# Kernel tuning notes

Hardware: AMD Instinct MI355X
Metric: run time of the kernel (lower is better)

The kernel has to match this reference:

```python
import jax, jax.numpy as jnp
import numpy as np

# HistogramQuantizer(percentile=99.99, gamma=0.99, n_bits=8, eps=0.0, act_decay=0.01), training mode
PERCENTILE = 99.99 / 100.0
GAMMA = 0.99
Q_MAX = float(2 ** (8 - 1) - 1)  # 127.0
EPS = 0.0
CLAMP_INIT = 100.0  # registered buffer initial value


def setup_inputs() -> dict:
    key = jax.random.key(0)
    x = jax.random.normal(key, (4, 4096, 4096), dtype=jnp.float32)
    return {"x": x}


def reference(x):
    x_abs = jnp.abs(x)
    # --- training-path percentile via full sort (quantile_from_sorted) ---
    flat = jnp.sort(x_abs.ravel())
    n = flat.size  # static
    k = int(round(PERCENTILE * n)) - 1
    clamp_value = flat[k]
    # EMA buffer update (side state; returned so the sort is not dead code)
    new_buffer = CLAMP_INIT * GAMMA + clamp_value * (1.0 - GAMMA)
    # --- fake quantization (Quantizer.forward with q_max=Q_MAX) ---
    # note: x_max/clamp_value only affects the backward mask, not the forward math
    scale = Q_MAX / jnp.maximum(jnp.max(x_abs), EPS)
    out = jnp.clip(jnp.round(x * scale), -Q_MAX, Q_MAX) / scale
    return out, new_buffer
```

## Files before the change

kernel.cpp:

```cpp
#include <hip/hip_runtime.h>
#include <math.h>

#define WS_MAXBITS 0
#define WS_SELBIN  1
#define WS_RANK    2
#define WS_HIST    4
#define HIST_WORDS 4096
#define WS_BMAX    4100
#define WS_CNT     5124
#define WS_CAND    6160
#define NBLK       1024
#define CAP        256

typedef float floatx4 __attribute__((ext_vector_type(4)));

extern "C" __global__ void __launch_bounds__(256)
k_max_hist(const float* __restrict__ x, long n, unsigned int* __restrict__ ws) {
    __shared__ unsigned int lhist[HIST_WORDS];
    __shared__ unsigned int wred[4];
    for (int i = threadIdx.x; i < HIST_WORDS; i += 256) lhist[i] = 0;
    __syncthreads();

    long n4 = n >> 2;
    const float4* x4 = (const float4*)x;
    unsigned int mymax = 0;
    long stride = (long)gridDim.x * 256;
    long i = (long)blockIdx.x * 256 + threadIdx.x;
    for (; i + stride < n4; i += 2 * stride) {
        float4 v0 = x4[i];
        float4 v1 = x4[i + stride];
        unsigned int a0 = __float_as_uint(fabsf(v0.x));
        unsigned int a1 = __float_as_uint(fabsf(v0.y));
        unsigned int a2 = __float_as_uint(fabsf(v0.z));
        unsigned int a3 = __float_as_uint(fabsf(v0.w));
        unsigned int b0 = __float_as_uint(fabsf(v1.x));
        unsigned int b1 = __float_as_uint(fabsf(v1.y));
        unsigned int b2 = __float_as_uint(fabsf(v1.z));
        unsigned int b3 = __float_as_uint(fabsf(v1.w));
        mymax = max(mymax, max(max(a0, a1), max(a2, a3)));
        mymax = max(mymax, max(max(b0, b1), max(b2, b3)));
        atomicAdd(&lhist[a0 >> 20], 1u);
        atomicAdd(&lhist[a1 >> 20], 1u);
        atomicAdd(&lhist[a2 >> 20], 1u);
        atomicAdd(&lhist[a3 >> 20], 1u);
        atomicAdd(&lhist[b0 >> 20], 1u);
        atomicAdd(&lhist[b1 >> 20], 1u);
        atomicAdd(&lhist[b2 >> 20], 1u);
        atomicAdd(&lhist[b3 >> 20], 1u);
    }
    for (; i < n4; i += stride) {
        float4 v = x4[i];
        unsigned int a0 = __float_as_uint(fabsf(v.x));
        unsigned int a1 = __float_as_uint(fabsf(v.y));
        unsigned int a2 = __float_as_uint(fabsf(v.z));
        unsigned int a3 = __float_as_uint(fabsf(v.w));
        mymax = max(mymax, max(max(a0, a1), max(a2, a3)));
        atomicAdd(&lhist[a0 >> 20], 1u);
        atomicAdd(&lhist[a1 >> 20], 1u);
        atomicAdd(&lhist[a2 >> 20], 1u);
        atomicAdd(&lhist[a3 >> 20], 1u);
    }
    if (blockIdx.x == 0 && threadIdx.x < (int)(n & 3)) {
        unsigned int a = __float_as_uint(fabsf(x[n4 * 4 + threadIdx.x]));
        mymax = max(mymax, a);
        atomicAdd(&lhist[a >> 20], 1u);
    }

    for (int off = 32; off > 0; off >>= 1)
        mymax = max(mymax, __shfl_down(mymax, off, 64));
    int lane = threadIdx.x & 63, wid = threadIdx.x >> 6;
    if (lane == 0) wred[wid] = mymax;
    __syncthreads();
    if (threadIdx.x == 0) {
        ws[WS_BMAX + blockIdx.x] =
            max(max(wred[0], wred[1]), max(wred[2], wred[3]));
    }
    unsigned int rot = (blockIdx.x * 1297u) & (HIST_WORDS - 1);
    for (int idx = threadIdx.x; idx < HIST_WORDS; idx += 256) {
        unsigned int bin = (idx + rot) & (HIST_WORDS - 1);
        unsigned int c = lhist[bin];
        if (c) atomicAdd(&ws[WS_HIST + bin], c);
    }
}

extern "C" __global__ void __launch_bounds__(256)
k_scan(unsigned int* __restrict__ ws, long k) {
    __shared__ unsigned long long partial[256];
    __shared__ unsigned int mred[256];
    const unsigned int* hist = ws + WS_HIST;

    unsigned int m = 0;
    for (int s = threadIdx.x; s < NBLK; s += 256) m = max(m, ws[WS_BMAX + s]);
    mred[threadIdx.x] = m;

    int base = threadIdx.x * (HIST_WORDS / 256);
    unsigned long long s = 0;
    for (int i = 0; i < 16; i++) s += hist[base + i];
    partial[threadIdx.x] = s;
    __syncthreads();
    if (threadIdx.x == 0) {
        unsigned int mm = 0;
        for (int t = 0; t < 256; t++) mm = max(mm, mred[t]);
        ws[WS_MAXBITS] = mm;

        unsigned long long acc = 0;
        long bin = -1;
        unsigned long long before = 0;
        for (int t = 0; t < 256; t++) {
            unsigned long long ps = partial[t];
            if (bin < 0 && acc + ps > (unsigned long long)k) {
                unsigned long long a2 = acc;
                for (int i = 0; i < 16; i++) {
                    unsigned int c = hist[t * 16 + i];
                    if (a2 + c > (unsigned long long)k) { bin = t * 16 + i; before = a2; break; }
                    a2 += c;
                }
            }
            acc += ps;
        }
        ws[WS_SELBIN] = (unsigned int)bin;
        ws[WS_RANK]   = (unsigned int)((unsigned long long)k - before);
    }
}

extern "C" __global__ void __launch_bounds__(256)
k_quant(const float* __restrict__ x, float* __restrict__ out, long n,
        unsigned int* __restrict__ ws) {
    __shared__ unsigned int lbuf[CAP];
    __shared__ unsigned int lcnt;
    if (threadIdx.x == 0) lcnt = 0;
    __syncthreads();

    float xmax = __uint_as_float(ws[WS_MAXBITS]);
    unsigned int selbin = ws[WS_SELBIN];
    float scale = 127.0f / xmax;
    float inv = 1.0f / scale;

    long n4 = n >> 2;
    const float4* x4 = (const float4*)x;
    floatx4* out4 = (floatx4*)out;
    long stride = (long)gridDim.x * 256;
    long i = (long)blockIdx.x * 256 + threadIdx.x;
    for (; i + stride < n4; i += 2 * stride) {
        float4 v0 = x4[i];
        float4 v1 = x4[i + stride];
        floatx4 r0, r1;
        r0.x = fminf(fmaxf(rintf(v0.x * scale), -127.0f), 127.0f) * inv;
        r0.y = fminf(fmaxf(rintf(v0.y * scale), -127.0f), 127.0f) * inv;
        r0.z = fminf(fmaxf(rintf(v0.z * scale), -127.0f), 127.0f) * inv;
        r0.w = fminf(fmaxf(rintf(v0.w * scale), -127.0f), 127.0f) * inv;
        r1.x = fminf(fmaxf(rintf(v1.x * scale), -127.0f), 127.0f) * inv;
        r1.y = fminf(fmaxf(rintf(v1.y * scale), -127.0f), 127.0f) * inv;
        r1.z = fminf(fmaxf(rintf(v1.z * scale), -127.0f), 127.0f) * inv;
        r1.w = fminf(fmaxf(rintf(v1.w * scale), -127.0f), 127.0f) * inv;
        __builtin_nontemporal_store(r0, &out4[i]);
        __builtin_nontemporal_store(r1, &out4[i + stride]);
        unsigned int a0 = __float_as_uint(fabsf(v0.x));
        unsigned int a1 = __float_as_uint(fabsf(v0.y));
        unsigned int a2 = __float_as_uint(fabsf(v0.z));
        unsigned int a3 = __float_as_uint(fabsf(v0.w));
        unsigned int b0 = __float_as_uint(fabsf(v1.x));
        unsigned int b1 = __float_as_uint(fabsf(v1.y));
        unsigned int b2 = __float_as_uint(fabsf(v1.z));
        unsigned int b3 = __float_as_uint(fabsf(v1.w));
        if ((a0 >> 20) == selbin) { unsigned int p = atomicAdd(&lcnt, 1u); if (p < CAP) lbuf[p] = a0; }
        if ((a1 >> 20) == selbin) { unsigned int p = atomicAdd(&lcnt, 1u); if (p < CAP) lbuf[p] = a1; }
        if ((a2 >> 20) == selbin) { unsigned int p = atomicAdd(&lcnt, 1u); if (p < CAP) lbuf[p] = a2; }
        if ((a3 >> 20) == selbin) { unsigned int p = atomicAdd(&lcnt, 1u); if (p < CAP) lbuf[p] = a3; }
        if ((b0 >> 20) == selbin) { unsigned int p = atomicAdd(&lcnt, 1u); if (p < CAP) lbuf[p] = b0; }
        if ((b1 >> 20) == selbin) { unsigned int p = atomicAdd(&lcnt, 1u); if (p < CAP) lbuf[p] = b1; }
        if ((b2 >> 20) == selbin) { unsigned int p = atomicAdd(&lcnt, 1u); if (p < CAP) lbuf[p] = b2; }
        if ((b3 >> 20) == selbin) { unsigned int p = atomicAdd(&lcnt, 1u); if (p < CAP) lbuf[p] = b3; }
    }
    for (; i < n4; i += stride) {
        float4 v = x4[i];
        floatx4 r;
        r.x = fminf(fmaxf(rintf(v.x * scale), -127.0f), 127.0f) * inv;
        r.y = fminf(fmaxf(rintf(v.y * scale), -127.0f), 127.0f) * inv;
        r.z = fminf(fmaxf(rintf(v.z * scale), -127.0f), 127.0f) * inv;
        r.w = fminf(fmaxf(rintf(v.w * scale), -127.0f), 127.0f) * inv;
        __builtin_nontemporal_store(r, &out4[i]);
        unsigned int a0 = __float_as_uint(fabsf(v.x));
        unsigned int a1 = __float_as_uint(fabsf(v.y));
        unsigned int a2 = __float_as_uint(fabsf(v.z));
        unsigned int a3 = __float_as_uint(fabsf(v.w));
        if ((a0 >> 20) == selbin) { unsigned int p = atomicAdd(&lcnt, 1u); if (p < CAP) lbuf[p] = a0; }
        if ((a1 >> 20) == selbin) { unsigned int p = atomicAdd(&lcnt, 1u); if (p < CAP) lbuf[p] = a1; }
        if ((a2 >> 20) == selbin) { unsigned int p = atomicAdd(&lcnt, 1u); if (p < CAP) lbuf[p] = a2; }
        if ((a3 >> 20) == selbin) { unsigned int p = atomicAdd(&lcnt, 1u); if (p < CAP) lbuf[p] = a3; }
    }
    if (blockIdx.x == 0 && threadIdx.x < (int)(n & 3)) {
        long t = n4 * 4 + threadIdx.x;
        float v = x[t];
        out[t] = fminf(fmaxf(rintf(v * scale), -127.0f), 127.0f) * inv;
        unsigned int a = __float_as_uint(fabsf(v));
        if ((a >> 20) == selbin) { unsigned int p = atomicAdd(&lcnt, 1u); if (p < CAP) lbuf[p] = a; }
    }
    __syncthreads();
    unsigned int c = lcnt; if (c > CAP) c = CAP;
    unsigned int* seg = ws + WS_CAND + (unsigned int)blockIdx.x * CAP;
    for (unsigned int e = threadIdx.x; e < c; e += 256) seg[e] = lbuf[e];
    if (threadIdx.x == 0) ws[WS_CNT + blockIdx.x] = c;
}

extern "C" __global__ void __launch_bounds__(256)
k_select(unsigned int* __restrict__ ws, float* __restrict__ out_last) {
    __shared__ unsigned int hist[1024];
    __shared__ unsigned int s_b1, s_j2;
    unsigned int j = ws[WS_RANK];
    unsigned int selbin = ws[WS_SELBIN];

    for (int i = threadIdx.x; i < 1024; i += 256) hist[i] = 0;
    __syncthreads();
    for (int s = threadIdx.x; s < NBLK; s += 256) {
        unsigned int c = ws[WS_CNT + s]; if (c > CAP) c = CAP;
        const unsigned int* seg = ws + WS_CAND + (unsigned int)s * CAP;
        for (unsigned int e = 0; e < c; e++)
            atomicAdd(&hist[(seg[e] >> 10) & 1023], 1u);
    }
    __syncthreads();
    if (threadIdx.x == 0) {
        unsigned int acc = 0, b1 = 1023;
        for (int b = 0; b < 1024; b++) {
            unsigned int h = hist[b];
            if (acc + h > j) { b1 = (unsigned int)b; break; }
            acc += h;
        }
        s_b1 = b1; s_j2 = j - acc;
    }
    __syncthreads();
    unsigned int pref = (selbin << 10) | s_b1;
    unsigned int j2 = s_j2;
    for (int i = threadIdx.x; i < 1024; i += 256) hist[i] = 0;
    __syncthreads();
    for (int s = threadIdx.x; s < NBLK; s += 256) {
        unsigned int c = ws[WS_CNT + s]; if (c > CAP) c = CAP;
        const unsigned int* seg = ws + WS_CAND + (unsigned int)s * CAP;
        for (unsigned int e = 0; e < c; e++) {
            unsigned int u = seg[e];
            if ((u >> 10) == pref) atomicAdd(&hist[u & 1023], 1u);
        }
    }
    __syncthreads();
    if (threadIdx.x == 0) {
        unsigned int acc = 0, b2 = 1023;
        for (int b = 0; b < 1024; b++) {
            unsigned int h = hist[b];
            if (acc + h > j2) { b2 = (unsigned int)b; break; }
            acc += h;
        }
        float clampv = __uint_as_float((pref << 10) | b2);
        out_last[0] = (float)(100.0 * 0.99 + (double)clampv * 0.01);
    }
}

extern "C" void kernel_launch(void* const* d_in, const int* in_sizes, int n_in,
                              void* d_out, int out_size, void* d_ws, size_t ws_size,
                              hipStream_t stream) {
    const float* x = (const float*)d_in[0];
    long n = (long)in_sizes[0];
    float* out = (float*)d_out;
    unsigned int* ws = (unsigned int*)d_ws;

    long k = (long)llround((99.99 / 100.0) * (double)n) - 1;
    if (k < 0) k = 0;
    if (k >= n) k = n - 1;

    (void)hipMemsetAsync((char*)d_ws + WS_HIST * sizeof(unsigned int), 0,
                         HIST_WORDS * sizeof(unsigned int), stream);

    k_max_hist<<<NBLK, 256, 0, stream>>>(x, n, ws);
    k_scan<<<1, 256, 0, stream>>>(ws, k);
    k_quant<<<NBLK, 256, 0, stream>>>(x, out, n, ws);
    k_select<<<1, 256, 0, stream>>>(ws, out + n);
}
```

Before: 589.7 us.

## Replace full histogram with sampled threshold and top-tail candidate selection

A small sampling kernel builds a coarse histogram of 256K elements to pick a conservative threshold T that places the 99.99th percentile in the tail above it. The first pass now computes max, counts elements above T and collects them as candidates, in place of doing a shared-memory atomic per element. The quant pass no longer filters candidates, and a three-level radix select runs over the compact candidate list. This removes per-element LDS atomics, at the cost of relying on the sample to bound the tail. Wrong T or candidate overflow (CAP, CANDMAX) could give an incorrect percentile.

```diff
diff --git a/kernel.cpp b/kernel.cpp
--- a/kernel.cpp
+++ b/kernel.cpp
@@ -1,138 +1,153 @@
 #include <hip/hip_runtime.h>
 #include <math.h>
 
+
 #define WS_MAXBITS 0
-#define WS_SELBIN  1
-#define WS_RANK    2
-#define WS_HIST    4
-#define HIST_WORDS 4096
-#define WS_BMAX    4100
-#define WS_CNT     5124
-#define WS_CAND    6160
+#define WS_NABOVE  1
+#define WS_CANDCNT 2
+#define WS_TBITS   3
+#define WS_SHIST   8
+#define SHIST_WORDS 4096
+#define WS_CAND    4104
+#define CANDMAX    262144
 #define NBLK       1024
-#define CAP        256
+#define CAP        512
 
 typedef float floatx4 __attribute__((ext_vector_type(4)));
 
 extern "C" __global__ void __launch_bounds__(256)
-k_max_hist(const float* __restrict__ x, long n, unsigned int* __restrict__ ws) {
-    __shared__ unsigned int lhist[HIST_WORDS];
-    __shared__ unsigned int wred[4];
-    for (int i = threadIdx.x; i < HIST_WORDS; i += 256) lhist[i] = 0;
-    __syncthreads();
+k_sample(const float* __restrict__ x, long n, unsigned int* __restrict__ ws) {
+    __shared__ unsigned int lh[SHIST_WORDS];
+    for (int i = threadIdx.x; i < SHIST_WORDS; i += 256) lh[i] = 0;
+    __syncthreads();
+    long seg = (n / 256) & ~3L;
+    long idx = (long)blockIdx.x * seg + (long)threadIdx.x * 4;
+    if (seg >= 4 && idx + 4 <= n) {
+        float4 v = *(const float4*)(x + idx);
+        unsigned int a0 = __float_as_uint(v.x) & 0x7fffffffu;
+        unsigned int a1 = __float_as_uint(v.y) & 0x7fffffffu;
+        unsigned int a2 = __float_as_uint(v.z) & 0x7fffffffu;
+        unsigned int a3 = __float_as_uint(v.w) & 0x7fffffffu;
+        atomicAdd(&lh[a0 >> 20], 1u);
+        atomicAdd(&lh[a1 >> 20], 1u);
+        atomicAdd(&lh[a2 >> 20], 1u);
+        atomicAdd(&lh[a3 >> 20], 1u);
+    }
+    __syncthreads();
+    unsigned int rot = (blockIdx.x * 1297u) & (SHIST_WORDS - 1);
+    for (int i = threadIdx.x; i < SHIST_WORDS; i += 256) {
+        unsigned int bin = (i + rot) & (SHIST_WORDS - 1);
+        unsigned int c = lh[bin];
+        if (c) atomicAdd(&ws[WS_SHIST + bin], c);
+    }
+}
+
+extern "C" __global__ void __launch_bounds__(256)
+k_thresh(unsigned int* __restrict__ ws, unsigned int C0) {
+    __shared__ unsigned int csum[256];
+    int tid = threadIdx.x;
+    const unsigned int* sh = ws + WS_SHIST;
+    unsigned int s = 0;
+    for (int i = 0; i < 16; i++) s += sh[tid * 16 + i];
+    csum[tid] = s;
+    __syncthreads();
+    unsigned int suf = 0;
+    for (int u = tid; u < 256; u++) suf += csum[u];
+    unsigned int sufnext = suf - s;
+    if (suf >= C0 && sufnext < C0) {
+        unsigned int acc = sufnext;
+        for (int i = 15; i >= 0; i--) {
+            acc += sh[tid * 16 + i];
+            if (acc >= C0) { ws[WS_TBITS] = ((unsigned int)(tid * 16 + i)) << 20; break; }
+        }
+    }
+    if (tid == 0 && suf < C0) ws[WS_TBITS] = 0u;
+}
+
+extern "C" __global__ void __launch_bounds__(256)
+k_pass1(const float* __restrict__ x, long n, unsigned int* __restrict__ ws) {
+    __shared__ unsigned int lbuf[CAP];
+    __shared__ unsigned int lcnt;
+    __shared__ unsigned int wred[4], wcnt[4], sbase[1];
+    if (threadIdx.x == 0) lcnt = 0;
+    __syncthreads();
+    unsigned int T = ws[WS_TBITS];
 
     long n4 = n >> 2;
     const float4* x4 = (const float4*)x;
-    unsigned int mymax = 0;
+    unsigned int mymax = 0, myc = 0;
     long stride = (long)gridDim.x * 256;
     long i = (long)blockIdx.x * 256 + threadIdx.x;
     for (; i + stride < n4; i += 2 * stride) {
         float4 v0 = x4[i];
         float4 v1 = x4[i + stride];
-        unsigned int a0 = __float_as_uint(fabsf(v0.x));
-        unsigned int a1 = __float_as_uint(fabsf(v0.y));
-        unsigned int a2 = __float_as_uint(fabsf(v0.z));
-        unsigned int a3 = __float_as_uint(fabsf(v0.w));
-        unsigned int b0 = __float_as_uint(fabsf(v1.x));
-        unsigned int b1 = __float_as_uint(fabsf(v1.y));
-        unsigned int b2 = __float_as_uint(fabsf(v1.z));
-        unsigned int b3 = __float_as_uint(fabsf(v1.w));
+        unsigned int a0 = __float_as_uint(v0.x) & 0x7fffffffu;
+        unsigned int a1 = __float_as_uint(v0.y) & 0x7fffffffu;
+        unsigned int a2 = __float_as_uint(v0.z) & 0x7fffffffu;
+        unsigned int a3 = __float_as_uint(v0.w) & 0x7fffffffu;
+        unsigned int b0 = __float_as_uint(v1.x) & 0x7fffffffu;
+        unsigned int b1 = __float_as_uint(v1.y) & 0x7fffffffu;
+        unsigned int b2 = __float_as_uint(v1.z) & 0x7fffffffu;
+        unsigned int b3 = __float_as_uint(v1.w) & 0x7fffffffu;
         mymax = max(mymax, max(max(a0, a1), max(a2, a3)));
         mymax = max(mymax, max(max(b0, b1), max(b2, b3)));
-        atomicAdd(&lhist[a0 >> 20], 1u);
-        atomicAdd(&lhist[a1 >> 20], 1u);
-        atomicAdd(&lhist[a2 >> 20], 1u);
-        atomicAdd(&lhist[a3 >> 20], 1u);
-        atomicAdd(&lhist[b0 >> 20], 1u);
-        atomicAdd(&lhist[b1 >> 20], 1u);
-        atomicAdd(&lhist[b2 >> 20], 1u);
-        atomicAdd(&lhist[b3 >> 20], 1u);
+        myc += (a0 > T) + (a1 > T) + (a2 > T) + (a3 > T);
+        myc += (b0 > T) + (b1 > T) + (b2 > T) + (b3 > T);
+        if (a0 > T) { unsigned int p = atomicAdd(&lcnt, 1u); if (p < CAP) lbuf[p] = a0; }
+        if (a1 > T) { unsigned int p = atomicAdd(&lcnt, 1u); if (p < CAP) lbuf[p] = a1; }
+        if (a2 > T) { unsigned int p = atomicAdd(&lcnt, 1u); if (p < CAP) lbuf[p] = a2; }
+        if (a3 > T) { unsigned int p = atomicAdd(&lcnt, 1u); if (p < CAP) lbuf[p] = a3; }
+        if (b0 > T) { unsigned int p = atomicAdd(&lcnt, 1u); if (p < CAP) lbuf[p] = b0; }
+        if (b1 > T) { unsigned int p = atomicAdd(&lcnt, 1u); if (p < CAP) lbuf[p] = b1; }
+        if (b2 > T) { unsigned int p = atomicAdd(&lcnt, 1u); if (p < CAP) lbuf[p] = b2; }
+        if (b3 > T) { unsigned int p = atomicAdd(&lcnt, 1u); if (p < CAP) lbuf[p] = b3; }
     }
     for (; i < n4; i += stride) {
         float4 v = x4[i];
-        unsigned int a0 = __float_as_uint(fabsf(v.x));
-        unsigned int a1 = __float_as_uint(fabsf(v.y));
-        unsigned int a2 = __float_as_uint(fabsf(v.z));
-        unsigned int a3 = __float_as_uint(fabsf(v.w));
+        unsigned int a0 = __float_as_uint(v.x) & 0x7fffffffu;
+        unsigned int a1 = __float_as_uint(v.y) & 0x7fffffffu;
+        unsigned int a2 = __float_as_uint(v.z) & 0x7fffffffu;
+        unsigned int a3 = __float_as_uint(v.w) & 0x7fffffffu;
         mymax = max(mymax, max(max(a0, a1), max(a2, a3)));
-        atomicAdd(&lhist[a0 >> 20], 1u);
-        atomicAdd(&lhist[a1 >> 20], 1u);
-        atomicAdd(&lhist[a2 >> 20], 1u);
-        atomicAdd(&lhist[a3 >> 20], 1u);
+        myc += (a0 > T) + (a1 > T) + (a2 > T) + (a3 > T);
+        if (a0 > T) { unsigned int p = atomicAdd(&lcnt, 1u); if (p < CAP) lbuf[p] = a0; }
+        if (a1 > T) { unsigned int p = atomicAdd(&lcnt, 1u); if (p < CAP) lbuf[p] = a1; }
+        if (a2 > T) { unsigned int p = atomicAdd(&lcnt, 1u); if (p < CAP) lbuf[p] = a2; }
+        if (a3 > T) { unsigned int p = atomicAdd(&lcnt, 1u); if (p < CAP) lbuf[p] = a3; }
     }
     if (blockIdx.x == 0 && threadIdx.x < (int)(n & 3)) {
-        unsigned int a = __float_as_uint(fabsf(x[n4 * 4 + threadIdx.x]));
+        unsigned int a = __float_as_uint(x[n4 * 4 + threadIdx.x]) & 0x7fffffffu;
         mymax = max(mymax, a);
-        atomicAdd(&lhist[a >> 20], 1u);
-    }
-
-    for (int off = 32; off > 0; off >>= 1)
+        myc += (a > T);
+        if (a > T) { unsigned int p = atomicAdd(&lcnt, 1u); if (p < CAP) lbuf[p] = a; }
+    }
+
+    for (int off = 32; off > 0; off >>= 1) {
         mymax = max(mymax, __shfl_down(mymax, off, 64));
+        myc += __shfl_down(myc, off, 64);
+    }
     int lane = threadIdx.x & 63, wid = threadIdx.x >> 6;
-    if (lane == 0) wred[wid] = mymax;
+    if (lane == 0) { wred[wid] = mymax; wcnt[wid] = myc; }
     __syncthreads();
     if (threadIdx.x == 0) {
-        ws[WS_BMAX + blockIdx.x] =
-            max(max(wred[0], wred[1]), max(wred[2], wred[3]));
-    }
-    unsigned int rot = (blockIdx.x * 1297u) & (HIST_WORDS - 1);
-    for (int idx = threadIdx.x; idx < HIST_WORDS; idx += 256) {
-        unsigned int bin = (idx + rot) & (HIST_WORDS - 1);
-        unsigned int c = lhist[bin];
-        if (c) atomicAdd(&ws[WS_HIST + bin], c);
-    }
-}
-
-extern "C" __global__ void __launch_bounds__(256)
-k_scan(unsigned int* __restrict__ ws, long k) {
-    __shared__ unsigned long long partial[256];
-    __shared__ unsigned int mred[256];
-    const unsigned int* hist = ws + WS_HIST;
-
-    unsigned int m = 0;
-    for (int s = threadIdx.x; s < NBLK; s += 256) m = max(m, ws[WS_BMAX + s]);
-    mred[threadIdx.x] = m;
-
-    int base = threadIdx.x * (HIST_WORDS / 256);
-    unsigned long long s = 0;
-    for (int i = 0; i < 16; i++) s += hist[base + i];
-    partial[threadIdx.x] = s;
-    __syncthreads();
-    if (threadIdx.x == 0) {
-        unsigned int mm = 0;
-        for (int t = 0; t < 256; t++) mm = max(mm, mred[t]);
-        ws[WS_MAXBITS] = mm;
-
-        unsigned long long acc = 0;
-        long bin = -1;
-        unsigned long long before = 0;
-        for (int t = 0; t < 256; t++) {
-            unsigned long long ps = partial[t];
-            if (bin < 0 && acc + ps > (unsigned long long)k) {
-                unsigned long long a2 = acc;
-                for (int i = 0; i < 16; i++) {
-                    unsigned int c = hist[t * 16 + i];
-                    if (a2 + c > (unsigned long long)k) { bin = t * 16 + i; before = a2; break; }
-                    a2 += c;
-                }
-            }
-            acc += ps;
-        }
-        ws[WS_SELBIN] = (unsigned int)bin;
-        ws[WS_RANK]   = (unsigned int)((unsigned long long)k - before);
-    }
+        unsigned int bm = max(max(wred[0], wred[1]), max(wred[2], wred[3]));
+        unsigned int bc = wcnt[0] + wcnt[1] + wcnt[2] + wcnt[3];
+        atomicMax(&ws[WS_MAXBITS], bm);
+        atomicAdd(&ws[WS_NABOVE], bc);
+        unsigned int c = lcnt; if (c > CAP) c = CAP;
+        wred[0] = c;
+        sbase[0] = atomicAdd(&ws[WS_CANDCNT], c);
+    }
+    __syncthreads();
+    unsigned int c = wred[0], base = sbase[0];
+    for (unsigned int e = threadIdx.x; e < c; e += 256)
+        if (base + e < CANDMAX) ws[WS_CAND + base + e] = lbuf[e];
 }
 
 extern "C" __global__ void __launch_bounds__(256)
 k_quant(const float* __restrict__ x, float* __restrict__ out, long n,
         unsigned int* __restrict__ ws) {
-    __shared__ unsigned int lbuf[CAP];
-    __shared__ unsigned int lcnt;
-    if (threadIdx.x == 0) lcnt = 0;
-    __syncthreads();
-
     float xmax = __uint_as_float(ws[WS_MAXBITS]);
-    unsigned int selbin = ws[WS_SELBIN];
     float scale = 127.0f / xmax;
     float inv = 1.0f / scale;
 
@@ -155,22 +170,6 @@
         r1.w = fminf(fmaxf(rintf(v1.w * scale), -127.0f), 127.0f) * inv;
         __builtin_nontemporal_store(r0, &out4[i]);
         __builtin_nontemporal_store(r1, &out4[i + stride]);
-        unsigned int a0 = __float_as_uint(fabsf(v0.x));
-        unsigned int a1 = __float_as_uint(fabsf(v0.y));
-        unsigned int a2 = __float_as_uint(fabsf(v0.z));
-        unsigned int a3 = __float_as_uint(fabsf(v0.w));
-        unsigned int b0 = __float_as_uint(fabsf(v1.x));
-        unsigned int b1 = __float_as_uint(fabsf(v1.y));
-        unsigned int b2 = __float_as_uint(fabsf(v1.z));
-        unsigned int b3 = __float_as_uint(fabsf(v1.w));
-        if ((a0 >> 20) == selbin) { unsigned int p = atomicAdd(&lcnt, 1u); if (p < CAP) lbuf[p] = a0; }
-        if ((a1 >> 20) == selbin) { unsigned int p = atomicAdd(&lcnt, 1u); if (p < CAP) lbuf[p] = a1; }
-        if ((a2 >> 20) == selbin) { unsigned int p = atomicAdd(&lcnt, 1u); if (p < CAP) lbuf[p] = a2; }
-        if ((a3 >> 20) == selbin) { unsigned int p = atomicAdd(&lcnt, 1u); if (p < CAP) lbuf[p] = a3; }
-        if ((b0 >> 20) == selbin) { unsigned int p = atomicAdd(&lcnt, 1u); if (p < CAP) lbuf[p] = b0; }
-        if ((b1 >> 20) == selbin) { unsigned int p = atomicAdd(&lcnt, 1u); if (p < CAP) lbuf[p] = b1; }
-        if ((b2 >> 20) == selbin) { unsigned int p = atomicAdd(&lcnt, 1u); if (p < CAP) lbuf[p] = b2; }
-        if ((b3 >> 20) == selbin) { unsigned int p = atomicAdd(&lcnt, 1u); if (p < CAP) lbuf[p] = b3; }
     }
     for (; i < n4; i += stride) {
         float4 v = x4[i];
@@ -180,76 +179,99 @@
         r.z = fminf(fmaxf(rintf(v.z * scale), -127.0f), 127.0f) * inv;
         r.w = fminf(fmaxf(rintf(v.w * scale), -127.0f), 127.0f) * inv;
         __builtin_nontemporal_store(r, &out4[i]);
-        unsigned int a0 = __float_as_uint(fabsf(v.x));
-        unsigned int a1 = __float_as_uint(fabsf(v.y));
-        unsigned int a2 = __float_as_uint(fabsf(v.z));
-        unsigned int a3 = __float_as_uint(fabsf(v.w));
-        if ((a0 >> 20) == selbin) { unsigned int p = atomicAdd(&lcnt, 1u); if (p < CAP) lbuf[p] = a0; }
-        if ((a1 >> 20) == selbin) { unsigned int p = atomicAdd(&lcnt, 1u); if (p < CAP) lbuf[p] = a1; }
-        if ((a2 >> 20) == selbin) { unsigned int p = atomicAdd(&lcnt, 1u); if (p < CAP) lbuf[p] = a2; }
-        if ((a3 >> 20) == selbin) { unsigned int p = atomicAdd(&lcnt, 1u); if (p < CAP) lbuf[p] = a3; }
     }
     if (blockIdx.x == 0 && threadIdx.x < (int)(n & 3)) {
         long t = n4 * 4 + threadIdx.x;
-        float v = x[t];
-        out[t] = fminf(fmaxf(rintf(v * scale), -127.0f), 127.0f) * inv;
-        unsigned int a = __float_as_uint(fabsf(v));
-        if ((a >> 20) == selbin) { unsigned int p = atomicAdd(&lcnt, 1u); if (p < CAP) lbuf[p] = a; }
-    }
-    __syncthreads();
-    unsigned int c = lcnt; if (c > CAP) c = CAP;
-    unsigned int* seg = ws + WS_CAND + (unsigned int)blockIdx.x * CAP;
-    for (unsigned int e = threadIdx.x; e < c; e += 256) seg[e] = lbuf[e];
-    if (threadIdx.x == 0) ws[WS_CNT + blockIdx.x] = c;
-}
-
-extern "C" __global__ void __launch_bounds__(256)
-k_select(unsigned int* __restrict__ ws, float* __restrict__ out_last) {
-    __shared__ unsigned int hist[1024];
-    __shared__ unsigned int s_b1, s_j2;
-    unsigned int j = ws[WS_RANK];
-    unsigned int selbin = ws[WS_SELBIN];
-
-    for (int i = threadIdx.x; i < 1024; i += 256) hist[i] = 0;
-    __syncthreads();
-    for (int s = threadIdx.x; s < NBLK; s += 256) {
-        unsigned int c = ws[WS_CNT + s]; if (c > CAP) c = CAP;
-        const unsigned int* seg = ws + WS_CAND + (unsigned int)s * CAP;
-        for (unsigned int e = 0; e < c; e++)
-            atomicAdd(&hist[(seg[e] >> 10) & 1023], 1u);
-    }
-    __syncthreads();
-    if (threadIdx.x == 0) {
-        unsigned int acc = 0, b1 = 1023;
-        for (int b = 0; b < 1024; b++) {
-            unsigned int h = hist[b];
-            if (acc + h > j) { b1 = (unsigned int)b; break; }
-            acc += h;
+        out[t] = fminf(fmaxf(rintf(x[t] * scale), -127.0f), 127.0f) * inv;
+    }
+}
+
+__device__ __forceinline__ void find_bin(const unsigned int* bins, int per,
+                                         unsigned int j, unsigned int* sfind,
+                                         unsigned int& out_b, unsigned int& out_jrem) {
+    int tid = threadIdx.x, lane = tid & 63, wid = tid >> 6;
+    unsigned int s = 0;
+    for (int i = 0; i < per; i++) s += bins[tid * per + i];
+    unsigned int inc = s;
+    for (int off = 1; off < 64; off <<= 1) {
+        unsigned int t = __shfl_up(inc, off, 64);
+        if (lane >= off) inc += t;
+    }
+    if (lane == 63) sfind[wid] = inc;
+    __syncthreads();
+    unsigned int wbase = 0;
+    for (int w = 0; w < wid; w++) wbase += sfind[w];
+    unsigned int excl = wbase + inc - s;
+    if (j >= excl && j < excl + s) {
+        unsigned int acc = excl;
+        for (int i = 0; i < per; i++) {
+            unsigned int c = bins[tid * per + i];
+            if (acc + c > j) { sfind[4] = (unsigned int)(tid * per + i); sfind[5] = j - acc; break; }
+            acc += c;
         }
-        s_b1 = b1; s_j2 = j - acc;
-    }
-    __syncthreads();
-    unsigned int pref = (selbin << 10) | s_b1;
-    unsigned int j2 = s_j2;
-    for (int i = threadIdx.x; i < 1024; i += 256) hist[i] = 0;
-    __syncthreads();
-    for (int s = threadIdx.x; s < NBLK; s += 256) {
-        unsigned int c = ws[WS_CNT + s]; if (c > CAP) c = CAP;
-        const unsigned int* seg = ws + WS_CAND + (unsigned int)s * CAP;
-        for (unsigned int e = 0; e < c; e++) {
-            unsigned int u = seg[e];
-            if ((u >> 10) == pref) atomicAdd(&hist[u & 1023], 1u);
-        }
-    }
-    __syncthreads();
-    if (threadIdx.x == 0) {
-        unsigned int acc = 0, b2 = 1023;
-        for (int b = 0; b < 1024; b++) {
-            unsigned int h = hist[b];
-            if (acc + h > j2) { b2 = (unsigned int)b; break; }
-            acc += h;
-        }
-        float clampv = __uint_as_float((pref << 10) | b2);
+    }
+    __syncthreads();
+    out_b = sfind[4];
+    out_jrem = sfind[5];
+    __syncthreads();
+}
+
+extern "C" __global__ void __launch_bounds__(256)
+k_select(unsigned int* __restrict__ ws, float* __restrict__ out_last, long r) {
+    __shared__ unsigned int h8[8 * 1025];
+    __shared__ unsigned int hm[1024];
+    __shared__ unsigned int h2[2048];
+    __shared__ unsigned int h3[1024];
+    __shared__ unsigned int sfind[8];
+    int tid = threadIdx.x;
+    if (tid < 8) sfind[tid] = 0;
+
+    unsigned int m = ws[WS_NABOVE];
+    unsigned int mc = ws[WS_CANDCNT]; if (mc > CANDMAX) mc = CANDMAX;
+    long jl = (long)m - 1 - r; if (jl < 0) jl = 0;
+    unsigned int j = (unsigned int)jl;
+    const unsigned int* cand = ws + WS_CAND;
+
+    for (int i = tid; i < 8 * 1025; i += 256) h8[i] = 0;
+    __syncthreads();
+    unsigned int rep = (unsigned int)(tid & 7) * 1025u;
+    for (unsigned int i = tid; i < mc; i += 256)
+        atomicAdd(&h8[rep + (cand[i] >> 21)], 1u);
+    __syncthreads();
+    for (int b = tid; b < 1024; b += 256) {
+        unsigned int s = 0;
+        for (int c = 0; c < 8; c++) s += h8[c * 1025 + b];
+        hm[b] = s;
+    }
+    __syncthreads();
+    unsigned int b1, j2;
+    find_bin(hm, 4, j, sfind, b1, j2);
+
+    for (int i = tid; i < 2048; i += 256) h2[i] = 0;
+    __syncthreads();
+    for (unsigned int i = tid; i < mc; i += 256) {
+        unsigned int u = cand[i];
+        if ((u >> 21) == b1) atomicAdd(&h2[(u >> 10) & 2047u], 1u);
+    }
+    __syncthreads();
+    unsigned int b2, j3;
+    find_bin(h2, 8, j2, sfind, b2, j3);
+
+    unsigned int pref = (b1 << 11) | b2;
+    for (int i = tid; i < 1024; i += 256) h3[i] = 0;
+    __syncthreads();
+    for (unsigned int i = tid; i < mc; i += 256) {
+        unsigned int u = cand[i];
+        if ((u >> 10) == pref) atomicAdd(&h3[u & 1023u], 1u);
+    }
+    __syncthreads();
+    unsigned int b3, j4;
+    find_bin(h3, 4, j3, sfind, b3, j4);
+    (void)j4;
+
+    if (tid == 0) {
+        unsigned int ans = (b1 << 21) | (b2 << 10) | b3;
+        float clampv = __uint_as_float(ans);
         out_last[0] = (float)(100.0 * 0.99 + (double)clampv * 0.01);
     }
 }
@@ -265,12 +287,17 @@
     long k = (long)llround((99.99 / 100.0) * (double)n) - 1;
     if (k < 0) k = 0;
     if (k >= n) k = n - 1;
-
-    (void)hipMemsetAsync((char*)d_ws + WS_HIST * sizeof(unsigned int), 0,
-                         HIST_WORDS * sizeof(unsigned int), stream);
-
-    k_max_hist<<<NBLK, 256, 0, stream>>>(x, n, ws);
-    k_scan<<<1, 256, 0, stream>>>(ws, k);
+    long r = n - 1 - k;
+
+    unsigned int C0 = (unsigned int)(4.0 * (double)(r + 1) * 262144.0 / (double)n) + 1u;
+    if (C0 < 64u) C0 = 64u;
+
+    (void)hipMemsetAsync(d_ws, 0, (WS_SHIST + SHIST_WORDS) * sizeof(unsigned int),
+                         stream);
+
+    k_sample<<<256, 256, 0, stream>>>(x, n, ws);
+    k_thresh<<<1, 256, 0, stream>>>(ws, C0);
+    k_pass1<<<NBLK, 256, 0, stream>>>(x, n, ws);
     k_quant<<<NBLK, 256, 0, stream>>>(x, out, n, ws);
-    k_select<<<1, 256, 0, stream>>>(ws, out + n);
-}
+    k_select<<<1, 256, 0, stream>>>(ws, out + n, r);
+}
```

After: 590.3 us. About the same (+0.1%).
